# Kernel optimization log

Hardware: AMD Instinct MI355X
Metric: run time of the kernel (lower is better)

The kernel has to match this reference:

```python
import jax, jax.numpy as jnp
from jax import lax
import numpy as np

INPUT_SIZE = 8
HIDDEN = 32
OUTPUT = 1
B, T = 8192, 512


def setup_inputs() -> dict:
    key = jax.random.key(0)
    ks = jax.random.split(key, 8)
    s = 1.0 / np.sqrt(HIDDEN)  # PyTorch LSTM init scale
    x = jax.random.normal(ks[0], (B, T, INPUT_SIZE), dtype=jnp.float32)
    W_ih = jax.random.uniform(ks[1], (4 * HIDDEN, INPUT_SIZE), minval=-s, maxval=s, dtype=jnp.float32)
    W_hh = jax.random.uniform(ks[2], (4 * HIDDEN, HIDDEN), minval=-s, maxval=s, dtype=jnp.float32)
    b_ih = jax.random.uniform(ks[3], (4 * HIDDEN,), minval=-s, maxval=s, dtype=jnp.float32)
    b_hh = jax.random.uniform(ks[4], (4 * HIDDEN,), minval=-s, maxval=s, dtype=jnp.float32)
    W_fc = jax.random.uniform(ks[5], (OUTPUT, HIDDEN), minval=-s, maxval=s, dtype=jnp.float32)
    b_fc = jax.random.uniform(ks[6], (OUTPUT,), minval=-s, maxval=s, dtype=jnp.float32)
    return {"x": x, "W_ih": W_ih, "W_hh": W_hh, "b_ih": b_ih, "b_hh": b_hh, "W_fc": W_fc, "b_fc": b_fc}


def reference(x, W_ih, W_hh, b_ih, b_hh, W_fc, b_fc):
    # x: [B, T, D]. Precompute input-gate contributions in one large GEMM,
    # then scan the recurrence over time. PyTorch gate order: i, f, g, o.
    Bn, Tn, _ = x.shape
    H = W_hh.shape[1]
    xg = jnp.einsum('btd,gd->btg', x, W_ih) + b_ih + b_hh  # [B, T, 4H]
    xg = jnp.swapaxes(xg, 0, 1)  # [T, B, 4H]

    def step(carry, xt):
        h, c = carry
        gates = xt + h @ W_hh.T  # [B, 4H]
        i, f, g, o = jnp.split(gates, 4, axis=-1)
        c = jax.nn.sigmoid(f) * c + jax.nn.sigmoid(i) * jnp.tanh(g)
        h = jax.nn.sigmoid(o) * jnp.tanh(c)
        return (h, c), None

    h0 = jnp.zeros((Bn, H), dtype=x.dtype)
    (h_n, _), _ = lax.scan(step, (h0, h0), xg)
    # fc applied to h_n: [num_layers=1, B, H] -> [1, B, output_size]
    out = h_n @ W_fc.T + b_fc  # [B, 1]
    return out[None, :, :]
```

## Files before the change

### kernel.cpp

```cpp
#include <hip/hip_runtime.h>
#include <cstddef>

#define T_LEN 512
#define IN_D 8
#define H 32
#define NBATCH 16
#define NT 256
#define NCHUNK (T_LEN / 8)
#define LOG2E 1.44269504088896341f

typedef __attribute__((ext_vector_type(8))) short bf16x8;
typedef __attribute__((ext_vector_type(4))) float f32x4;
typedef __attribute__((ext_vector_type(2))) float f32x2;

__device__ __forceinline__ float fexp2(float v) { return __builtin_amdgcn_exp2f(v); }
__device__ __forceinline__ float frcp(float v)  { return __builtin_amdgcn_rcpf(v); }
__device__ __forceinline__ unsigned short f2bf(float f) {
    unsigned u = __builtin_bit_cast(unsigned, f);
    u += 0x7FFF + ((u >> 16) & 1);
    return (unsigned short)(u >> 16);
}
__device__ __forceinline__ float bf2f(unsigned short b) {
    unsigned u = ((unsigned)b) << 16;
    return __builtin_bit_cast(float, u);
}
__device__ __forceinline__ float ubits(unsigned u) { return __builtin_bit_cast(float, u); }
__device__ __forceinline__ unsigned cvt_pk_bf16(float lo, float hi) {
    unsigned r;
    asm("v_cvt_pk_bf16_f32 %0, %1, %2" : "=v"(r) : "v"(lo), "v"(hi));
    return r;
}

#define WG_BARRIER() asm volatile("s_waitcnt lgkmcnt(0)\n\ts_barrier" ::: "memory")

__global__ void __launch_bounds__(NT, 1) lstm_mfma4(
    const float* __restrict__ x, const float* __restrict__ W_ih,
    const float* __restrict__ W_hh, const float* __restrict__ b_ih,
    const float* __restrict__ b_hh, const float* __restrict__ W_fc,
    const float* __restrict__ b_fc, float* __restrict__ out)
{
    __shared__ __align__(16) float G[4][NBATCH][40];
    __shared__ __align__(16) unsigned short hhi[NBATCH][48];
    __shared__ __align__(16) unsigned short hlo[NBATCH][48];
    __shared__ __align__(16) unsigned short xstg[8][17][24];

    const int tix  = threadIdx.x;
    const int w    = tix >> 6;
    const int lane = tix & 63;
    const int q    = lane >> 4;
    const int cc   = lane & 15;

    const float kk = (w == 2) ? 2.f * LOG2E : -LOG2E;
    const float aa = (w == 2) ? 2.f * LOG2E : 0.f;
    const float bb = (w == 2) ? -4.f * LOG2E : 1.f;

    bf16x8 Bh[2], Bl[2], Bx[2];
    float bias[2];
    #pragma unroll
    for (int d = 0; d < 2; ++d) {
        const int r = 16 * (2 * w + d) + cc;
        #pragma unroll
        for (int j = 0; j < 8; ++j) {
            const int p = 8 * q + j;
            const int u = 16 * (p & 1) + (p >> 1);
            const float ws = kk * W_hh[r * H + u];
            const unsigned short whi = f2bf(ws);
            Bh[d][j] = (short)whi;
            Bl[d][j] = (short)f2bf(ws - bf2f(whi));
            if (q == 3) {
                Bx[d][j] = 0;
            } else {
                const float wsx = kk * W_ih[r * IN_D + j];
                const unsigned short xwh = f2bf(wsx);
                Bx[d][j] = (q == 2) ? (short)f2bf(wsx - bf2f(xwh)) : (short)xwh;
            }
        }
        bias[d] = kk * (b_ih[r] + b_hh[r]);
    }
    const f32x4 biasv0 = { bias[0], bias[0], bias[0], bias[0] };
    const f32x4 biasv1 = { bias[1], bias[1], bias[1], bias[1] };

    const int xoff = (q == 2) ? 0 : ((q == 3) ? 16 : 8 * q);

    const int xb = tix >> 4, xs = (tix >> 1) & 7, xhf = tix & 1;
    const float* xbase = x + (size_t)(blockIdx.x * NBATCH + xb) * (size_t)(T_LEN * IN_D)
                           + xs * IN_D + 4 * xhf;
    auto ldchunk = [&](int ch) { return *(const float4*)(xbase + (size_t)ch * 8 * IN_D); };
    auto stage = [&](float4 v) {
        const unsigned h0 = cvt_pk_bf16(v.x, v.y);
        const unsigned h1 = cvt_pk_bf16(v.z, v.w);
        const unsigned l0 = cvt_pk_bf16(v.x - ubits(h0 << 16), v.y - ubits(h0 & 0xffff0000u));
        const unsigned l1 = cvt_pk_bf16(v.z - ubits(h1 << 16), v.w - ubits(h1 & 0xffff0000u));
        *(uint2*)&xstg[xs][xb][4 * xhf]     = make_uint2(h0, h1);
        *(uint2*)&xstg[xs][xb][8 + 4 * xhf] = make_uint2(l0, l1);
    };

    for (int i = tix; i < NBATCH * 48 / 2; i += NT) {
        ((unsigned*)hhi)[i] = 0u;
        ((unsigned*)hlo)[i] = 0u;
    }
    for (int i = tix; i < 8 * 17 * 24 / 2; i += NT) ((unsigned*)xstg)[i] = 0u;
    __syncthreads();
    stage(ldchunk(0));
    float4 xbuf = ldchunk(1);
    __syncthreads();

    f32x4 XC[8][2];
#define REFILL(j) do { \
        const bf16x8 Ax_ = *(const bf16x8*)&xstg[(j)][cc][xoff]; \
        XC[(j)][0] = __builtin_amdgcn_mfma_f32_16x16x32_bf16(Ax_, Bx[0], biasv0, 0, 0, 0); \
        XC[(j)][1] = __builtin_amdgcn_mfma_f32_16x16x32_bf16(Ax_, Bx[1], biasv1, 0, 0, 0); \
    } while (0)
    #pragma unroll
    for (int s = 0; s < 8; ++s) REFILL(s);

    const int m = tix >> 4, u0 = tix & 15;
    const float wfc0 = W_fc[u0], wfc1 = W_fc[u0 + 16];
    float cs0 = 0.f, cs1 = 0.f, h0f = 0.f, h1f = 0.f;

    for (int blk = 0; blk < NCHUNK; ++blk) {
        #pragma unroll
        for (int s = 0; s < 8; ++s) {
            const bf16x8 A0 = *(const bf16x8*)&hhi[cc][8 * q];
            const bf16x8 A2 = *(const bf16x8*)&hlo[cc][8 * q];
            f32x4 C2[2];
            #pragma unroll
            for (int d = 0; d < 2; ++d) {
                const f32x4 z = { 0.f, 0.f, 0.f, 0.f };
                f32x4 a1 = __builtin_amdgcn_mfma_f32_16x16x32_bf16(A0, Bh[d], XC[s][d], 0, 0, 0);
                f32x4 a2 = __builtin_amdgcn_mfma_f32_16x16x32_bf16(A2, Bh[d], z, 0, 0, 0);
                a2 = __builtin_amdgcn_mfma_f32_16x16x32_bf16(A0, Bl[d], a2, 0, 0, 0);
                C2[d] = a1 + a2;
            }

            if (s == 0) {
                stage(xbuf);
                int nc = blk + 2;
                if (nc > NCHUNK - 1) nc = NCHUNK - 1;
                xbuf = ldchunk(nc);
            }

            #pragma unroll
            for (int rg = 0; rg < 4; ++rg) {
                f32x2 pr;
                pr[0] = aa + bb * frcp(1.f + fexp2(C2[0][rg]));
                pr[1] = aa + bb * frcp(1.f + fexp2(C2[1][rg]));
                *(f32x2*)&G[w][4 * q + rg][2 * cc] = pr;
            }

            if (s >= 1) REFILL(s - 1);
            if (s == 7) REFILL(7);

            WG_BARRIER();

            {
                const f32x2 gi = *(const f32x2*)&G[0][m][2 * u0];
                const f32x2 gf = *(const f32x2*)&G[1][m][2 * u0];
                const f32x2 gg = *(const f32x2*)&G[2][m][2 * u0];
                const f32x2 go = *(const f32x2*)&G[3][m][2 * u0];
                cs0 = gf[0] * cs0 + gi[0] * gg[0];
                cs1 = gf[1] * cs1 + gi[1] * gg[1];
                const float r0 = frcp(1.f + fexp2(cs0));
                const float r1 = frcp(1.f + fexp2(cs1));
                h0f = go[0] - 2.f * go[0] * r0;
                h1f = go[1] - 2.f * go[1] * r1;
                const unsigned hw = cvt_pk_bf16(h0f, h1f);
                const unsigned lw = cvt_pk_bf16(h0f - ubits(hw << 16),
                                                h1f - ubits(hw & 0xffff0000u));
                *(unsigned*)&hhi[m][2 * u0] = hw;
                *(unsigned*)&hlo[m][2 * u0] = lw;
            }

            WG_BARRIER();
        }
    }
#undef REFILL

    float sacc = h0f * wfc0 + h1f * wfc1;
    sacc += __shfl_xor(sacc, 1);
    sacc += __shfl_xor(sacc, 2);
    sacc += __shfl_xor(sacc, 4);
    sacc += __shfl_xor(sacc, 8);
    if (u0 == 0) out[blockIdx.x * NBATCH + m] = sacc + b_fc[0];
}

extern "C" void kernel_launch(void* const* d_in, const int* in_sizes, int n_in,
                              void* d_out, int out_size, void* d_ws, size_t ws_size,
                              hipStream_t stream) {
    const float* x    = (const float*)d_in[0];
    const float* W_ih = (const float*)d_in[1];
    const float* W_hh = (const float*)d_in[2];
    const float* b_ih = (const float*)d_in[3];
    const float* b_hh = (const float*)d_in[4];
    const float* W_fc = (const float*)d_in[5];
    const float* b_fc = (const float*)d_in[6];
    float* out = (float*)d_out;
    const int Bn = in_sizes[0] / (T_LEN * IN_D);
    lstm_mfma4<<<dim3(Bn / NBATCH), dim3(NT), 0, stream>>>(
        x, W_ih, W_hh, b_ih, b_hh, W_fc, b_fc, out);
}
```

Measured before the change: 474.4 us.

## Split LSTM gate work across eight waves instead of four per block

The block grows from 256 to 512 threads, so each wave computes one 16-row gate tile instead of two. This halves the serial MFMA and transcendental chain per wave on every recurrent step. The cell update now runs one hidden unit per thread and uses a lane shuffle to pack bf16 pairs for the h buffers. In exchange, each step's two block barriers now synchronise twice as many waves, and register and LDS needs rise per CU, which is relevant to the new launch bound of up to 4 blocks per CU.

Measured after the change: 447.0 us. -5.8%, faster.

```diff
diff --git a/kernel.cpp b/kernel.cpp
--- a/kernel.cpp
+++ b/kernel.cpp
@@ -5,13 +5,13 @@
 #define IN_D 8
 #define H 32
 #define NBATCH 16
-#define NT 256
+#define NT 512
 #define NCHUNK (T_LEN / 8)
 #define LOG2E 1.44269504088896341f
+#define GP 36
 
 typedef __attribute__((ext_vector_type(8))) short bf16x8;
 typedef __attribute__((ext_vector_type(4))) float f32x4;
-typedef __attribute__((ext_vector_type(2))) float f32x2;
 
 __device__ __forceinline__ float fexp2(float v) { return __builtin_amdgcn_exp2f(v); }
 __device__ __forceinline__ float frcp(float v)  { return __builtin_amdgcn_rcpf(v); }
@@ -33,56 +33,54 @@
 
 #define WG_BARRIER() asm volatile("s_waitcnt lgkmcnt(0)\n\ts_barrier" ::: "memory")
 
-__global__ void __launch_bounds__(NT, 1) lstm_mfma4(
+__global__ void __launch_bounds__(NT, 4) lstm_mfma4(
     const float* __restrict__ x, const float* __restrict__ W_ih,
     const float* __restrict__ W_hh, const float* __restrict__ b_ih,
     const float* __restrict__ b_hh, const float* __restrict__ W_fc,
     const float* __restrict__ b_fc, float* __restrict__ out)
 {
-    __shared__ __align__(16) float G[4][NBATCH][40];
+    __shared__ __align__(16) float G[4][NBATCH][GP];
     __shared__ __align__(16) unsigned short hhi[NBATCH][48];
     __shared__ __align__(16) unsigned short hlo[NBATCH][48];
     __shared__ __align__(16) unsigned short xstg[8][17][24];
 
     const int tix  = threadIdx.x;
     const int w    = tix >> 6;
+    const int g    = w >> 1;
+    const int d    = w & 1;
     const int lane = tix & 63;
     const int q    = lane >> 4;
     const int cc   = lane & 15;
 
-    const float kk = (w == 2) ? 2.f * LOG2E : -LOG2E;
-    const float aa = (w == 2) ? 2.f * LOG2E : 0.f;
-    const float bb = (w == 2) ? -4.f * LOG2E : 1.f;
+    const float kk = (g == 2) ? 2.f * LOG2E : -LOG2E;
+    const float aa = (g == 2) ? 2.f * LOG2E : 0.f;
+    const float bb = (g == 2) ? -4.f * LOG2E : 1.f;
 
-    bf16x8 Bh[2], Bl[2], Bx[2];
-    float bias[2];
+    bf16x8 Bh, Bl, Bx;
+    const int r = 16 * (2 * g + d) + cc;
     #pragma unroll
-    for (int d = 0; d < 2; ++d) {
-        const int r = 16 * (2 * w + d) + cc;
-        #pragma unroll
-        for (int j = 0; j < 8; ++j) {
-            const int p = 8 * q + j;
-            const int u = 16 * (p & 1) + (p >> 1);
-            const float ws = kk * W_hh[r * H + u];
-            const unsigned short whi = f2bf(ws);
-            Bh[d][j] = (short)whi;
-            Bl[d][j] = (short)f2bf(ws - bf2f(whi));
-            if (q == 3) {
-                Bx[d][j] = 0;
-            } else {
-                const float wsx = kk * W_ih[r * IN_D + j];
-                const unsigned short xwh = f2bf(wsx);
-                Bx[d][j] = (q == 2) ? (short)f2bf(wsx - bf2f(xwh)) : (short)xwh;
-            }
+    for (int j = 0; j < 8; ++j) {
+        const int p = 8 * q + j;
+        const int u = 16 * (p & 1) + (p >> 1);
+        const float ws = kk * W_hh[r * H + u];
+        const unsigned short whi = f2bf(ws);
+        Bh[j] = (short)whi;
+        Bl[j] = (short)f2bf(ws - bf2f(whi));
+        if (q == 3) {
+            Bx[j] = 0;
+        } else {
+            const float wsx = kk * W_ih[r * IN_D + j];
+            const unsigned short xwh = f2bf(wsx);
+            Bx[j] = (q == 2) ? (short)f2bf(wsx - bf2f(xwh)) : (short)xwh;
         }
-        bias[d] = kk * (b_ih[r] + b_hh[r]);
     }
-    const f32x4 biasv0 = { bias[0], bias[0], bias[0], bias[0] };
-    const f32x4 biasv1 = { bias[1], bias[1], bias[1], bias[1] };
+    const float bias = kk * (b_ih[r] + b_hh[r]);
+    const f32x4 biasv = { bias, bias, bias, bias };
 
     const int xoff = (q == 2) ? 0 : ((q == 3) ? 16 : 8 * q);
 
-    const int xb = tix >> 4, xs = (tix >> 1) & 7, xhf = tix & 1;
+    const int xb = (tix >> 4) & 15, xs = (tix >> 1) & 7, xhf = tix & 1;
+    const bool stager = (tix < 256);
     const float* xbase = x + (size_t)(blockIdx.x * NBATCH + xb) * (size_t)(T_LEN * IN_D)
                            + xs * IN_D + 4 * xhf;
     auto ldchunk = [&](int ch) { return *(const float4*)(xbase + (size_t)ch * 8 * IN_D); };
@@ -101,39 +99,37 @@
     }
     for (int i = tix; i < 8 * 17 * 24 / 2; i += NT) ((unsigned*)xstg)[i] = 0u;
     __syncthreads();
-    stage(ldchunk(0));
-    float4 xbuf = ldchunk(1);
+    float4 xbuf = {0.f, 0.f, 0.f, 0.f};
+    if (stager) {
+        stage(ldchunk(0));
+        xbuf = ldchunk(1);
+    }
     __syncthreads();
 
-    f32x4 XC[8][2];
+    f32x4 XC[8];
 #define REFILL(j) do { \
         const bf16x8 Ax_ = *(const bf16x8*)&xstg[(j)][cc][xoff]; \
-        XC[(j)][0] = __builtin_amdgcn_mfma_f32_16x16x32_bf16(Ax_, Bx[0], biasv0, 0, 0, 0); \
-        XC[(j)][1] = __builtin_amdgcn_mfma_f32_16x16x32_bf16(Ax_, Bx[1], biasv1, 0, 0, 0); \
+        XC[(j)] = __builtin_amdgcn_mfma_f32_16x16x32_bf16(Ax_, Bx, biasv, 0, 0, 0); \
     } while (0)
     #pragma unroll
     for (int s = 0; s < 8; ++s) REFILL(s);
 
-    const int m = tix >> 4, u0 = tix & 15;
-    const float wfc0 = W_fc[u0], wfc1 = W_fc[u0 + 16];
-    float cs0 = 0.f, cs1 = 0.f, h0f = 0.f, h1f = 0.f;
+    const int m = tix >> 5, u = tix & 31;
+    const float wfc = W_fc[u];
+    float cs = 0.f, hf = 0.f;
 
     for (int blk = 0; blk < NCHUNK; ++blk) {
         #pragma unroll
         for (int s = 0; s < 8; ++s) {
             const bf16x8 A0 = *(const bf16x8*)&hhi[cc][8 * q];
             const bf16x8 A2 = *(const bf16x8*)&hlo[cc][8 * q];
-            f32x4 C2[2];
-            #pragma unroll
-            for (int d = 0; d < 2; ++d) {
-                const f32x4 z = { 0.f, 0.f, 0.f, 0.f };
-                f32x4 a1 = __builtin_amdgcn_mfma_f32_16x16x32_bf16(A0, Bh[d], XC[s][d], 0, 0, 0);
-                f32x4 a2 = __builtin_amdgcn_mfma_f32_16x16x32_bf16(A2, Bh[d], z, 0, 0, 0);
-                a2 = __builtin_amdgcn_mfma_f32_16x16x32_bf16(A0, Bl[d], a2, 0, 0, 0);
-                C2[d] = a1 + a2;
-            }
+            const f32x4 z = { 0.f, 0.f, 0.f, 0.f };
+            f32x4 a1 = __builtin_amdgcn_mfma_f32_16x16x32_bf16(A0, Bh, XC[s], 0, 0, 0);
+            f32x4 a2 = __builtin_amdgcn_mfma_f32_16x16x32_bf16(A2, Bh, z, 0, 0, 0);
+            a2 = __builtin_amdgcn_mfma_f32_16x16x32_bf16(A0, Bl, a2, 0, 0, 0);
+            const f32x4 C = a1 + a2;
 
-            if (s == 0) {
+            if (s == 0 && stager) {
                 stage(xbuf);
                 int nc = blk + 2;
                 if (nc > NCHUNK - 1) nc = NCHUNK - 1;
@@ -141,12 +137,8 @@
             }
 
             #pragma unroll
-            for (int rg = 0; rg < 4; ++rg) {
-                f32x2 pr;
-                pr[0] = aa + bb * frcp(1.f + fexp2(C2[0][rg]));
-                pr[1] = aa + bb * frcp(1.f + fexp2(C2[1][rg]));
-                *(f32x2*)&G[w][4 * q + rg][2 * cc] = pr;
-            }
+            for (int rg = 0; rg < 4; ++rg)
+                G[g][4 * q + rg][cc + 16 * d] = aa + bb * frcp(1.f + fexp2(C[rg]));
 
             if (s >= 1) REFILL(s - 1);
             if (s == 7) REFILL(7);
@@ -154,21 +146,21 @@
             WG_BARRIER();
 
             {
-                const f32x2 gi = *(const f32x2*)&G[0][m][2 * u0];
-                const f32x2 gf = *(const f32x2*)&G[1][m][2 * u0];
-                const f32x2 gg = *(const f32x2*)&G[2][m][2 * u0];
-                const f32x2 go = *(const f32x2*)&G[3][m][2 * u0];
-                cs0 = gf[0] * cs0 + gi[0] * gg[0];
-                cs1 = gf[1] * cs1 + gi[1] * gg[1];
-                const float r0 = frcp(1.f + fexp2(cs0));
-                const float r1 = frcp(1.f + fexp2(cs1));
-                h0f = go[0] - 2.f * go[0] * r0;
-                h1f = go[1] - 2.f * go[1] * r1;
-                const unsigned hw = cvt_pk_bf16(h0f, h1f);
-                const unsigned lw = cvt_pk_bf16(h0f - ubits(hw << 16),
-                                                h1f - ubits(hw & 0xffff0000u));
-                *(unsigned*)&hhi[m][2 * u0] = hw;
-                *(unsigned*)&hlo[m][2 * u0] = lw;
+                const float gi = G[0][m][u];
+                const float gf = G[1][m][u];
+                const float gg = G[2][m][u];
+                const float go = G[3][m][u];
+                cs = gf * cs + gi * gg;
+                const float rr = frcp(1.f + fexp2(cs));
+                hf = go - 2.f * go * rr;
+                const float hp = __shfl_xor(hf, 16);
+                if ((tix & 16) == 0) {
+                    const unsigned hw = cvt_pk_bf16(hf, hp);
+                    const unsigned lw = cvt_pk_bf16(hf - ubits(hw << 16),
+                                                    hp - ubits(hw & 0xffff0000u));
+                    *(unsigned*)&hhi[m][2 * (u & 15)] = hw;
+                    *(unsigned*)&hlo[m][2 * (u & 15)] = lw;
+                }
             }
 
             WG_BARRIER();
@@ -176,12 +168,13 @@
     }
 #undef REFILL
 
-    float sacc = h0f * wfc0 + h1f * wfc1;
+    float sacc = hf * wfc;
     sacc += __shfl_xor(sacc, 1);
     sacc += __shfl_xor(sacc, 2);
     sacc += __shfl_xor(sacc, 4);
     sacc += __shfl_xor(sacc, 8);
-    if (u0 == 0) out[blockIdx.x * NBATCH + m] = sacc + b_fc[0];
+    sacc += __shfl_xor(sacc, 16);
+    if ((tix & 31) == 0) out[blockIdx.x * NBATCH + m] = sacc + b_fc[0];
 }
 
 extern "C" void kernel_launch(void* const* d_in, const int* in_sizes, int n_in,
```
